# Performance work log

Hardware: AMD Instinct MI355X
Metric: run time of the kernel (lower is better)

## Reference

```python
import jax, jax.numpy as jnp
import numpy as np

N_NODES = 100000


def gcn_conv(x, edge_index, W, b):
    # PyG GCNConv: add self-loops, symmetric normalization, then scatter-add.
    n = x.shape[0]
    loops = jnp.arange(n, dtype=edge_index.dtype)
    src = jnp.concatenate([edge_index[0], loops])
    dst = jnp.concatenate([edge_index[1], loops])
    h = x @ W  # [N, F_out] -- transform before propagate (small GEMM)
    ones = jnp.ones(src.shape[0], dtype=x.dtype)
    deg = jax.ops.segment_sum(ones, dst, num_segments=n)  # in-degree incl. self-loop
    dinv = jnp.where(deg > 0, jax.lax.rsqrt(deg), 0.0)
    norm = dinv[src] * dinv[dst]  # [E+N]
    msg = h[src] * norm[:, None]  # gather + scale, [E+N, F_out]
    out = jax.ops.segment_sum(msg, dst, num_segments=n)  # scatter-add
    return out + b


def setup_inputs() -> dict:
    key = jax.random.key(0)
    k1, k2, k3, k4 = jax.random.split(key, 4)
    d = 128
    x = jax.random.normal(k1, (N_NODES, d), dtype=jnp.float32)
    edge_index = jax.random.randint(k2, (2, 1600000), 0, N_NODES, dtype=jnp.int64)
    scale = 1.0 / np.sqrt(d)
    W1 = jax.random.normal(k3, (d, d), dtype=jnp.float32) * scale
    b1 = jnp.zeros((d,), dtype=jnp.float32)
    W2 = jax.random.normal(k4, (d, d), dtype=jnp.float32) * scale
    b2 = jnp.zeros((d,), dtype=jnp.float32)
    return {"x": x, "edge_index": edge_index, "W1": W1, "b1": b1, "W2": W2, "b2": b2}


def reference(x, edge_index, W1, b1, W2, b2):
    # Layer 1: GCNConv -> relu -> dropout(eval: identity)
    h = jax.nn.relu(gcn_conv(x, edge_index, W1, b1))
    # Layer 2
    h = jax.nn.relu(gcn_conv(h, edge_index, W2, b2))
    return h
```

## Files before the change

### kernel.cpp

```cpp
#include <hip/hip_runtime.h>


#define NFEAT 128
#define BSH 7
#define MAXNB 1024
#define BCAP 4096
#define HP 72
#define YP 132
#define CH2 2048

typedef __attribute__((ext_vector_type(8))) short s8v;
typedef __attribute__((ext_vector_type(4))) float f4v;
typedef __attribute__((ext_vector_type(2))) float f2v;
typedef __attribute__((ext_vector_type(4))) uint u4v;

__device__ inline ushort f2bf(float f) {
    union { float f; uint u; } x; x.f = f;
    uint u = x.u;
    return (ushort)((u + 0x7fffu + ((u >> 16) & 1u)) >> 16);
}
__device__ inline f2v unpk(uint u) {
    union { uint u; float f; } lo, hi;
    lo.u = u << 16;
    hi.u = u & 0xffff0000u;
    return (f2v){lo.f, hi.f};
}
__device__ inline void upfma2(uint4 v, float g, f2v* a) {
    a[0] += g * unpk(v.x);
    a[1] += g * unpk(v.y);
    a[2] += g * unpk(v.z);
    a[3] += g * unpk(v.w);
}

__device__ inline void node_gather(const uint4* __restrict__ hs4,
                                   const int* __restrict__ row_ptr,
                                   const int* __restrict__ col,
                                   const float* __restrict__ dinv,
                                   int node, int sub, f2v* a) {
    uint4 vself = hs4[(size_t)node * 16 + sub];
    float dself = dinv[node];
    int s = row_ptr[node], e = row_ptr[node + 1];
    int nb = (e - s) >> 2;
    int k = s;
    if (nb > 0) {
        int c0 = col[k], c1 = col[k + 1], c2 = col[k + 2], c3 = col[k + 3];
        uint4 v0 = hs4[(size_t)c0 * 16 + sub];
        uint4 v1 = hs4[(size_t)c1 * 16 + sub];
        uint4 v2 = hs4[(size_t)c2 * 16 + sub];
        uint4 v3 = hs4[(size_t)c3 * 16 + sub];
        float g0 = dinv[c0], g1 = dinv[c1], g2 = dinv[c2], g3 = dinv[c3];
        int d0 = col[k + 4], d1 = col[k + 5], d2 = col[k + 6], d3 = col[k + 7];
        k += 8;
        upfma2(vself, dself, a);
        for (int it = 1; it < nb; ++it, k += 4) {
            uint4 w0 = hs4[(size_t)d0 * 16 + sub];
            uint4 w1 = hs4[(size_t)d1 * 16 + sub];
            uint4 w2 = hs4[(size_t)d2 * 16 + sub];
            uint4 w3 = hs4[(size_t)d3 * 16 + sub];
            float h0 = dinv[d0], h1 = dinv[d1], h2 = dinv[d2], h3 = dinv[d3];
            int t0 = col[k], t1 = col[k + 1], t2 = col[k + 2], t3 = col[k + 3];
            upfma2(v0, g0, a); upfma2(v1, g1, a); upfma2(v2, g2, a); upfma2(v3, g3, a);
            v0 = w0; v1 = w1; v2 = w2; v3 = w3;
            g0 = h0; g1 = h1; g2 = h2; g3 = h3;
            d0 = t0; d1 = t1; d2 = t2; d3 = t3;
        }
        upfma2(v0, g0, a); upfma2(v1, g1, a); upfma2(v2, g2, a); upfma2(v3, g3, a);
        k = s + nb * 4;
    } else {
        upfma2(vself, dself, a);
    }
    for (; k < e; ++k) {
        int c = col[k];
        upfma2(hs4[(size_t)c * 16 + sub], dinv[c], a);
    }
}

__device__ inline void stage_w_half(ushort* Bs, const float* __restrict__ W, int h, int t) {
#pragma unroll
    for (int i = 0; i < 8; i++) {
        int idx = t + i * 256;
        int k4 = idx >> 7;
        int n = idx & 127;
        ushort o[4];
#pragma unroll
        for (int j = 0; j < 4; j++) o[j] = f2bf(W[(h * 64 + k4 * 4 + j) * NFEAT + n]);
        uint2 pk;
        __builtin_memcpy(&pk, o, 8);
        *(uint2*)&Bs[n * HP + k4 * 4] = pk;
    }
}

__global__ __launch_bounds__(256) void k_bsort(const int* __restrict__ src,
                                               const int* __restrict__ dst,
                                               int* __restrict__ gcnt,
                                               uint* __restrict__ ebuf,
                                               int E, int NB) {
    __shared__ int cnt_[MAXNB];
    __shared__ int loff[MAXNB];
    __shared__ int gbase[MAXNB];
    __shared__ int wpart[4];
    __shared__ uint sv[CH2];
    __shared__ ushort sb[CH2];

    int t = threadIdx.x;
    int e0 = blockIdx.x * CH2;
    int m = min(CH2, E - e0);

#pragma unroll
    for (int i = t; i < MAXNB; i += 256) cnt_[i] = 0;
    __syncthreads();
    for (int e = e0 + t; e < e0 + m; e += 256) atomicAdd(&cnt_[dst[e] >> BSH], 1);
    __syncthreads();
    for (int b = t; b < NB; b += 256) {
        int c = cnt_[b];
        gbase[b] = c ? (b * BCAP + atomicAdd(&gcnt[b], c)) : 0;
    }
    int v0 = cnt_[t * 4], v1 = cnt_[t * 4 + 1], v2 = cnt_[t * 4 + 2], v3 = cnt_[t * 4 + 3];
    int my = v0 + v1 + v2 + v3;
    int lane = t & 63, wv = t >> 6;
    int sc = my;
#pragma unroll
    for (int off = 1; off < 64; off <<= 1) {
        int up = __shfl_up(sc, off, 64);
        if (lane >= off) sc += up;
    }
    if (lane == 63) wpart[wv] = sc;
    __syncthreads();
    int wbase = 0;
    for (int j = 0; j < wv; j++) wbase += wpart[j];
    int run = wbase + sc - my;
    loff[t * 4] = run; cnt_[t * 4] = run; run += v0;
    loff[t * 4 + 1] = run; cnt_[t * 4 + 1] = run; run += v1;
    loff[t * 4 + 2] = run; cnt_[t * 4 + 2] = run; run += v2;
    loff[t * 4 + 3] = run; cnt_[t * 4 + 3] = run;
    __syncthreads();
    for (int e = e0 + t; e < e0 + m; e += 256) {
        int d = dst[e];
        int b = d >> BSH;
        int p = atomicAdd(&cnt_[b], 1);
        sv[p] = ((uint)src[e] << BSH) | (uint)(d & ((1 << BSH) - 1));
        sb[p] = (ushort)b;
    }
    __syncthreads();
    for (int i = t; i < m; i += 256) {
        int b = sb[i];
        int slot = gbase[b] + (i - loff[b]);
        if (slot < (b + 1) * BCAP) ebuf[slot] = sv[i];
    }
}

template <bool ABF16>
__device__ inline void gemm_body(ushort* Bs, int bid, const void* __restrict__ Ap,
                                 const float* __restrict__ W,
                                 ushort* __restrict__ hs, int M) {
    int t = threadIdx.x;
    int w = t >> 6, l = t & 63;
    int q = l >> 4, ln = l & 15;
    int row0 = (bid * 4 + w) * 16;

    int arow = row0 + ln;
    if (arow >= M) arow = M - 1;
    s8v afr[4];
    if (ABF16) {
        const ushort* A = (const ushort*)Ap + (size_t)arow * NFEAT + q * 8;
#pragma unroll
        for (int g = 0; g < 4; g++) afr[g] = *(const s8v*)(A + g * 32);
    } else {
        const float* A = (const float*)Ap + (size_t)arow * NFEAT + q * 8;
#pragma unroll
        for (int g = 0; g < 4; g++) {
            float4 f0 = *(const float4*)(A + g * 32);
            float4 f1 = *(const float4*)(A + g * 32 + 4);
            ushort o[8] = {f2bf(f0.x), f2bf(f0.y), f2bf(f0.z), f2bf(f0.w),
                           f2bf(f1.x), f2bf(f1.y), f2bf(f1.z), f2bf(f1.w)};
            __builtin_memcpy(&afr[g], o, 16);
        }
    }

    f4v acc[8];
#pragma unroll
    for (int nt = 0; nt < 8; nt++) acc[nt] = (f4v){0.f, 0.f, 0.f, 0.f};

#pragma unroll
    for (int h = 0; h < 2; h++) {
        if (h) __syncthreads();
        stage_w_half(Bs, W, h, t);
        __syncthreads();
#pragma unroll
        for (int nt = 0; nt < 8; nt++) {
            const ushort* Bp = Bs + (nt * 16 + ln) * HP + q * 8;
#pragma unroll
            for (int ks = 0; ks < 2; ks++) {
                s8v bfr = *(const s8v*)(Bp + ks * 32);
                acc[nt] = __builtin_amdgcn_mfma_f32_16x16x32_bf16(afr[h * 2 + ks], bfr, acc[nt], 0, 0, 0);
            }
        }
    }

#pragma unroll
    for (int r = 0; r < 4; r++) {
        int row = row0 + q * 4 + r;
        if (row < M) {
            ushort* hp = hs + (size_t)row * NFEAT + ln;
#pragma unroll
            for (int nt = 0; nt < 8; nt++) hp[nt * 16] = f2bf(acc[nt][r]);
        }
    }
}

__device__ inline void fill2_body(char* smem, int b,
                                  const uint* __restrict__ ebuf,
                                  const int* __restrict__ gcnt,
                                  int* __restrict__ row_ptr,
                                  float* __restrict__ dinv,
                                  int* __restrict__ col,
                                  int N, int E, int NB) {
    int* cnt = (int*)smem;
    int* pre = cnt + 128;
    int* sred = pre + 128;
    int* colL = sred + 256;
    int t = threadIdx.x;
    int part = 0;
    for (int j = t; j < b; j += 256) part += gcnt[j];
#pragma unroll
    for (int off = 32; off >= 1; off >>= 1) part += __shfl_down(part, off, 64);
    if ((t & 63) == 0) sred[t >> 6] = part;
    __syncthreads();
    int gb = sred[0] + sred[1] + sred[2] + sred[3];
    int m = min(gcnt[b], BCAP);
    if (t < 128) cnt[t] = 0;
    __syncthreads();
    const uint* eb = ebuf + (size_t)b * BCAP;
    for (int i = t; i < m; i += 256) atomicAdd(&cnt[eb[i] & 127], 1);
    __syncthreads();
    if (t < 128) pre[t] = cnt[t];
    __syncthreads();
    for (int off = 1; off < 128; off <<= 1) {
        int add = (t >= off && t < 128) ? pre[t - off] : 0;
        __syncthreads();
        if (t < 128) pre[t] += add;
        __syncthreads();
    }
    if (t < 128) {
        pre[t] -= cnt[t];
        int node = (b << BSH) + t;
        if (node < N) {
            row_ptr[node] = gb + pre[t];
            dinv[node] = rsqrtf((float)(cnt[t] + 1));
        }
    }
    __syncthreads();
    for (int i = t; i < m; i += 256) {
        uint p = eb[i];
        int pos = atomicAdd(&pre[p & 127], 1);
        colL[pos] = (int)(p >> BSH);
    }
    __syncthreads();
    for (int i = t; i < m; i += 256) col[gb + i] = colL[i];
    if (b == NB - 1 && t == 0) row_ptr[N] = E;
}

__global__ __launch_bounds__(256) void k_fused2(const uint* __restrict__ ebuf,
                                                const int* __restrict__ gcnt,
                                                int* __restrict__ row_ptr,
                                                float* __restrict__ dinv,
                                                int* __restrict__ col,
                                                int N, int E, int NB,
                                                const float* __restrict__ x,
                                                const float* __restrict__ W1,
                                                ushort* __restrict__ hs) {
    __shared__ __align__(16) char smem[18432];
    int bid = blockIdx.x;
    int r = bid % 3;
    int fid = bid / 3;
    if (r == 0 && fid < NB) {
        fill2_body(smem, fid, ebuf, gcnt, row_ptr, dinv, col, N, E, NB);
    } else {
        int fills_before = min(fid + (r ? 1 : 0), NB);
        gemm_body<false>((ushort*)smem, bid - fills_before, x, W1, hs, N);
    }
}

__global__ __launch_bounds__(256, 4) void k_aggG(const uint4* __restrict__ hs4,
                                                 const int* __restrict__ row_ptr,
                                                 const int* __restrict__ col,
                                                 const float* __restrict__ dinv,
                                                 const float* __restrict__ bias,
                                                 const float* __restrict__ W2,
                                                 ushort* __restrict__ hs2, int N) {
    __shared__ __align__(16) ushort smem[128 * HP];
    ushort* yT = smem;
    ushort* Bs = smem;
    int t = threadIdx.x;
    int grp = t >> 4, sub = t & 15;
    int base = blockIdx.x * 64;

    const float4* b4 = (const float4*)bias;
    float4 bb0 = b4[sub * 2], bb1 = b4[sub * 2 + 1];

    for (int i = 0; i < 4; i++) {
        int myn = grp + i * 16;
        int node = base + myn;
        uint4 pk = make_uint4(0, 0, 0, 0);
        if (node < N) {
            f2v a[4];
#pragma unroll
            for (int j = 0; j < 4; j++) a[j] = (f2v){0.f, 0.f};
            node_gather(hs4, row_ptr, col, dinv, node, sub, a);
            float di = dinv[node];
            ushort o[8];
            o[0] = f2bf(fmaxf(fmaf(di, a[0].x, bb0.x), 0.f));
            o[1] = f2bf(fmaxf(fmaf(di, a[0].y, bb0.y), 0.f));
            o[2] = f2bf(fmaxf(fmaf(di, a[1].x, bb0.z), 0.f));
            o[3] = f2bf(fmaxf(fmaf(di, a[1].y, bb0.w), 0.f));
            o[4] = f2bf(fmaxf(fmaf(di, a[2].x, bb1.x), 0.f));
            o[5] = f2bf(fmaxf(fmaf(di, a[2].y, bb1.y), 0.f));
            o[6] = f2bf(fmaxf(fmaf(di, a[3].x, bb1.z), 0.f));
            o[7] = f2bf(fmaxf(fmaf(di, a[3].y, bb1.w), 0.f));
            __builtin_memcpy(&pk, o, 16);
        }
        *(uint4*)&yT[myn * YP + sub * 8] = pk;
    }
    __syncthreads();

    int w = t >> 6, l = t & 63;
    int q = l >> 4, ln = l & 15;
    s8v a2[4];
#pragma unroll
    for (int g = 0; g < 4; g++)
        a2[g] = *(const s8v*)&yT[(w * 16 + ln) * YP + g * 32 + q * 8];
    __syncthreads();

    f4v acc[8];
#pragma unroll
    for (int nt = 0; nt < 8; nt++) acc[nt] = (f4v){0.f, 0.f, 0.f, 0.f};
#pragma unroll
    for (int h = 0; h < 2; h++) {
        if (h) __syncthreads();
        stage_w_half(Bs, W2, h, t);
        __syncthreads();
#pragma unroll
        for (int nt = 0; nt < 8; nt++) {
            const ushort* Bp = Bs + (nt * 16 + ln) * HP + q * 8;
#pragma unroll
            for (int ks = 0; ks < 2; ks++) {
                s8v bfr = *(const s8v*)(Bp + ks * 32);
                acc[nt] = __builtin_amdgcn_mfma_f32_16x16x32_bf16(a2[h * 2 + ks], bfr, acc[nt], 0, 0, 0);
            }
        }
    }
#pragma unroll
    for (int rr = 0; rr < 4; rr++) {
        int node = base + w * 16 + q * 4 + rr;
        if (node < N) {
            ushort* hp = hs2 + (size_t)node * NFEAT + ln;
#pragma unroll
            for (int nt = 0; nt < 8; nt++) hp[nt * 16] = f2bf(acc[nt][rr]);
        }
    }
}

template <bool OUT_BF16>
__global__ __launch_bounds__(256) void k_aggregate(const uint4* __restrict__ hs4,
                                                   const int* __restrict__ row_ptr,
                                                   const int* __restrict__ col,
                                                   const float* __restrict__ dinv,
                                                   const float* __restrict__ bias,
                                                   void* __restrict__ outp, int N) {
    int node = blockIdx.x * 16 + (threadIdx.x >> 4);
    if (node >= N) return;
    int sub = threadIdx.x & 15;

    f2v a[4];
#pragma unroll
    for (int j = 0; j < 4; j++) a[j] = (f2v){0.f, 0.f};
    node_gather(hs4, row_ptr, col, dinv, node, sub, a);

    float di = dinv[node];
    const float4* b4 = (const float4*)bias;
    float4 b0 = b4[sub * 2], b1 = b4[sub * 2 + 1];
    float r[8];
    r[0] = fmaxf(fmaf(di, a[0].x, b0.x), 0.f);
    r[1] = fmaxf(fmaf(di, a[0].y, b0.y), 0.f);
    r[2] = fmaxf(fmaf(di, a[1].x, b0.z), 0.f);
    r[3] = fmaxf(fmaf(di, a[1].y, b0.w), 0.f);
    r[4] = fmaxf(fmaf(di, a[2].x, b1.x), 0.f);
    r[5] = fmaxf(fmaf(di, a[2].y, b1.y), 0.f);
    r[6] = fmaxf(fmaf(di, a[3].x, b1.z), 0.f);
    r[7] = fmaxf(fmaf(di, a[3].y, b1.w), 0.f);
    if (OUT_BF16) {
        ushort o[8];
#pragma unroll
        for (int j = 0; j < 8; j++) o[j] = f2bf(r[j]);
        u4v pk;
        __builtin_memcpy(&pk, o, 16);
        __builtin_nontemporal_store(pk, (u4v*)outp + (size_t)node * 16 + sub);
    } else {
        float* orow = (float*)outp + (size_t)node * NFEAT + sub * 8;
        f4v r0 = {r[0], r[1], r[2], r[3]};
        f4v r1 = {r[4], r[5], r[6], r[7]};
        __builtin_nontemporal_store(r0, (f4v*)orow);
        __builtin_nontemporal_store(r1, (f4v*)(orow + 4));
    }
}

extern "C" void kernel_launch(void* const* d_in, const int* in_sizes, int n_in,
                              void* d_out, int out_size, void* d_ws, size_t ws_size,
                              hipStream_t stream) {
    const float* x = (const float*)d_in[0];
    const int* ei = (const int*)d_in[1];
    const float* W1 = (const float*)d_in[2];
    const float* b1 = (const float*)d_in[3];
    const float* W2 = (const float*)d_in[4];
    const float* b2 = (const float*)d_in[5];
    float* out = (float*)d_out;

    const int N = in_sizes[0] / NFEAT;
    const int E = in_sizes[1] / 2;
    const int* src = ei;
    const int* dst = ei + E;
    const int NB = (N + (1 << BSH) - 1) >> BSH;

    char* w = (char*)d_ws;
    size_t off = 0;
    auto alloc = [&](size_t bytes) -> void* {
        void* p = w + off;
        off = (off + bytes + 511) & ~(size_t)511;
        return p;
    };
    ushort* hs = (ushort*)alloc((size_t)N * NFEAT * 2);
    ushort* hs2 = (ushort*)alloc((size_t)N * NFEAT * 2);
    int* row_ptr = (int*)alloc((size_t)(N + 1) * 4);
    float* dinv = (float*)alloc((size_t)N * 4);
    int* col = (int*)alloc((size_t)(E + 64) * 4);
    uint* ebuf = (uint*)alloc((size_t)NB * BCAP * 4);
    int* gcnt = (int*)alloc((size_t)MAXNB * 4);
    (void)ws_size; (void)n_in; (void)out_size;

    const int sortBlk = (E + CH2 - 1) / CH2;
    const int gemmBlk = (N + 63) / 64;
    const int aggBlk = (N + 15) / 16;

    hipMemsetAsync(gcnt, 0, (size_t)MAXNB * 4, stream);
    k_bsort<<<sortBlk, 256, 0, stream>>>(src, dst, gcnt, ebuf, E, NB);
    k_fused2<<<NB + gemmBlk, 256, 0, stream>>>(ebuf, gcnt, row_ptr, dinv, col, N, E, NB,
                                               x, W1, hs);
    k_aggG<<<gemmBlk, 256, 0, stream>>>((const uint4*)hs, row_ptr, col, dinv, b1, W2, hs2, N);
    k_aggregate<false><<<aggBlk, 256, 0, stream>>>((const uint4*)hs2, row_ptr, col, dinv, b2, out, N);
}
```

Measured before the change: 306.0 us.

## Drop global CSR build; sort bucket halves in LDS inside aggregation kernels

Removes the separate CSR fill pass (row_ptr, col, dinv) and instead has each aggregation block locally sort its half-bucket of edges into LDS, with a small atomic degree kernel feeding the source-side normalization. The source-side dinv scaling is folded into the GEMM epilogue, so the gather does plain adds with no per-neighbor dinv loads. The bucket sort now runs fused alongside the first GEMM. In exchange each of the two aggregation kernels re-reads and re-sorts ebuf, a global atomic degree pass is added, and per-half neighbor lists are capped at 2048 entries.

Result: slower. 357.9 us (+16.9%).

```diff
diff --git a/kernel.cpp b/kernel.cpp
--- a/kernel.cpp
+++ b/kernel.cpp
@@ -8,6 +8,7 @@
 #define HP 72
 #define YP 132
 #define CH2 2048
+#define CLCAP 2064
 
 typedef __attribute__((ext_vector_type(8))) short s8v;
 typedef __attribute__((ext_vector_type(4))) float f4v;
@@ -25,54 +26,81 @@
     hi.u = u & 0xffff0000u;
     return (f2v){lo.f, hi.f};
 }
-__device__ inline void upfma2(uint4 v, float g, f2v* a) {
-    a[0] += g * unpk(v.x);
-    a[1] += g * unpk(v.y);
-    a[2] += g * unpk(v.z);
-    a[3] += g * unpk(v.w);
-}
-
-__device__ inline void node_gather(const uint4* __restrict__ hs4,
-                                   const int* __restrict__ row_ptr,
-                                   const int* __restrict__ col,
-                                   const float* __restrict__ dinv,
-                                   int node, int sub, f2v* a) {
+__device__ inline void upadd2(uint4 v, f2v* a) {
+    a[0] += unpk(v.x);
+    a[1] += unpk(v.y);
+    a[2] += unpk(v.z);
+    a[3] += unpk(v.w);
+}
+
+__device__ inline void node_gather_lds(const uint4* __restrict__ hs4,
+                                       const int* colL, int s, int e,
+                                       int node, int sub, f2v* a) {
     uint4 vself = hs4[(size_t)node * 16 + sub];
-    float dself = dinv[node];
-    int s = row_ptr[node], e = row_ptr[node + 1];
     int nb = (e - s) >> 2;
     int k = s;
     if (nb > 0) {
-        int c0 = col[k], c1 = col[k + 1], c2 = col[k + 2], c3 = col[k + 3];
+        int c0 = colL[k], c1 = colL[k + 1], c2 = colL[k + 2], c3 = colL[k + 3];
         uint4 v0 = hs4[(size_t)c0 * 16 + sub];
         uint4 v1 = hs4[(size_t)c1 * 16 + sub];
         uint4 v2 = hs4[(size_t)c2 * 16 + sub];
         uint4 v3 = hs4[(size_t)c3 * 16 + sub];
-        float g0 = dinv[c0], g1 = dinv[c1], g2 = dinv[c2], g3 = dinv[c3];
-        int d0 = col[k + 4], d1 = col[k + 5], d2 = col[k + 6], d3 = col[k + 7];
+        int d0 = colL[k + 4], d1 = colL[k + 5], d2 = colL[k + 6], d3 = colL[k + 7];
         k += 8;
-        upfma2(vself, dself, a);
+        upadd2(vself, a);
         for (int it = 1; it < nb; ++it, k += 4) {
             uint4 w0 = hs4[(size_t)d0 * 16 + sub];
             uint4 w1 = hs4[(size_t)d1 * 16 + sub];
             uint4 w2 = hs4[(size_t)d2 * 16 + sub];
             uint4 w3 = hs4[(size_t)d3 * 16 + sub];
-            float h0 = dinv[d0], h1 = dinv[d1], h2 = dinv[d2], h3 = dinv[d3];
-            int t0 = col[k], t1 = col[k + 1], t2 = col[k + 2], t3 = col[k + 3];
-            upfma2(v0, g0, a); upfma2(v1, g1, a); upfma2(v2, g2, a); upfma2(v3, g3, a);
+            int t0 = colL[k], t1 = colL[k + 1], t2 = colL[k + 2], t3 = colL[k + 3];
+            upadd2(v0, a); upadd2(v1, a); upadd2(v2, a); upadd2(v3, a);
             v0 = w0; v1 = w1; v2 = w2; v3 = w3;
-            g0 = h0; g1 = h1; g2 = h2; g3 = h3;
             d0 = t0; d1 = t1; d2 = t2; d3 = t3;
         }
-        upfma2(v0, g0, a); upfma2(v1, g1, a); upfma2(v2, g2, a); upfma2(v3, g3, a);
+        upadd2(v0, a); upadd2(v1, a); upadd2(v2, a); upadd2(v3, a);
         k = s + nb * 4;
     } else {
-        upfma2(vself, dself, a);
-    }
-    for (; k < e; ++k) {
-        int c = col[k];
-        upfma2(hs4[(size_t)c * 16 + sub], dinv[c], a);
-    }
+        upadd2(vself, a);
+    }
+    for (; k < e; ++k) upadd2(hs4[(size_t)colL[k] * 16 + sub], a);
+}
+
+__device__ inline void half_sort(const uint* __restrict__ ebuf,
+                                 const int* __restrict__ gcnt,
+                                 int b, int half, int* cnt, int* sstart, int* pre,
+                                 int* colL) {
+    int t = threadIdx.x;
+    int m = min(gcnt[b], BCAP);
+    const uint* eb = ebuf + (size_t)b * BCAP;
+    if (t < 64) cnt[t] = 0;
+    __syncthreads();
+    for (int i = t; i < m; i += 256) {
+        int low = (int)(eb[i] & 127u);
+        if ((low >> 6) == half) atomicAdd(&cnt[low & 63], 1);
+    }
+    __syncthreads();
+    if (t < 64) {
+        int v = cnt[t];
+        int sc = v;
+#pragma unroll
+        for (int off = 1; off < 64; off <<= 1) {
+            int u = __shfl_up(sc, off, 64);
+            if (t >= off) sc += u;
+        }
+        sstart[t] = sc - v;
+        pre[t] = sc - v;
+    }
+    __syncthreads();
+    for (int i = t; i < m; i += 256) {
+        uint p = eb[i];
+        int low = (int)(p & 127u);
+        if ((low >> 6) == half) {
+            int pos = atomicAdd(&pre[low & 63], 1);
+            if (pos < 2048) colL[pos] = (int)(p >> BSH);
+        }
+    }
+    __syncthreads();
 }
 
 __device__ inline void stage_w_half(ushort* Bs, const float* __restrict__ W, int h, int t) {
@@ -90,20 +118,36 @@
     }
 }
 
-__global__ __launch_bounds__(256) void k_bsort(const int* __restrict__ src,
-                                               const int* __restrict__ dst,
-                                               int* __restrict__ gcnt,
-                                               uint* __restrict__ ebuf,
-                                               int E, int NB) {
-    __shared__ int cnt_[MAXNB];
-    __shared__ int loff[MAXNB];
-    __shared__ int gbase[MAXNB];
-    __shared__ int wpart[4];
-    __shared__ uint sv[CH2];
-    __shared__ ushort sb[CH2];
+__global__ __launch_bounds__(256) void k_deg(const int* __restrict__ dst,
+                                             int* __restrict__ deg, int E) {
+    int i = blockIdx.x * 256 + threadIdx.x;
+    int stride = gridDim.x * 256;
+    int E4 = E >> 2;
+    const int4* d4 = (const int4*)dst;
+    for (int k = i; k < E4; k += stride) {
+        int4 v = d4[k];
+        atomicAdd(&deg[v.x], 1);
+        atomicAdd(&deg[v.y], 1);
+        atomicAdd(&deg[v.z], 1);
+        atomicAdd(&deg[v.w], 1);
+    }
+    for (int k = E4 * 4 + i; k < E; k += stride) atomicAdd(&deg[dst[k]], 1);
+}
+
+__device__ inline void bsort_body(char* smem, int sid,
+                                  const int* __restrict__ src,
+                                  const int* __restrict__ dst,
+                                  int* __restrict__ gcnt,
+                                  uint* __restrict__ ebuf, int E, int NB) {
+    int* cnt_ = (int*)smem;
+    int* loff = cnt_ + MAXNB;
+    int* gbase = loff + MAXNB;
+    int* wpart = gbase + MAXNB;
+    uint* sv = (uint*)(wpart + 4);
+    ushort* sb = (ushort*)(sv + CH2);
 
     int t = threadIdx.x;
-    int e0 = blockIdx.x * CH2;
+    int e0 = sid * CH2;
     int m = min(CH2, E - e0);
 
 #pragma unroll
@@ -149,10 +193,10 @@
     }
 }
 
-template <bool ABF16>
-__device__ inline void gemm_body(ushort* Bs, int bid, const void* __restrict__ Ap,
-                                 const float* __restrict__ W,
-                                 ushort* __restrict__ hs, int M) {
+__device__ inline void gemm_body_f32(ushort* Bs, int bid, const float* __restrict__ Ap,
+                                     const float* __restrict__ W,
+                                     const int* __restrict__ deg,
+                                     ushort* __restrict__ hs, int M) {
     int t = threadIdx.x;
     int w = t >> 6, l = t & 63;
     int q = l >> 4, ln = l & 15;
@@ -161,20 +205,14 @@
     int arow = row0 + ln;
     if (arow >= M) arow = M - 1;
     s8v afr[4];
-    if (ABF16) {
-        const ushort* A = (const ushort*)Ap + (size_t)arow * NFEAT + q * 8;
-#pragma unroll
-        for (int g = 0; g < 4; g++) afr[g] = *(const s8v*)(A + g * 32);
-    } else {
-        const float* A = (const float*)Ap + (size_t)arow * NFEAT + q * 8;
-#pragma unroll
-        for (int g = 0; g < 4; g++) {
-            float4 f0 = *(const float4*)(A + g * 32);
-            float4 f1 = *(const float4*)(A + g * 32 + 4);
-            ushort o[8] = {f2bf(f0.x), f2bf(f0.y), f2bf(f0.z), f2bf(f0.w),
-                           f2bf(f1.x), f2bf(f1.y), f2bf(f1.z), f2bf(f1.w)};
-            __builtin_memcpy(&afr[g], o, 16);
-        }
+    const float* A = Ap + (size_t)arow * NFEAT + q * 8;
+#pragma unroll
+    for (int g = 0; g < 4; g++) {
+        float4 f0 = *(const float4*)(A + g * 32);
+        float4 f1 = *(const float4*)(A + g * 32 + 4);
+        ushort o[8] = {f2bf(f0.x), f2bf(f0.y), f2bf(f0.z), f2bf(f0.w),
+                       f2bf(f1.x), f2bf(f1.y), f2bf(f1.z), f2bf(f1.w)};
+        __builtin_memcpy(&afr[g], o, 16);
     }
 
     f4v acc[8];
@@ -201,113 +239,71 @@
     for (int r = 0; r < 4; r++) {
         int row = row0 + q * 4 + r;
         if (row < M) {
+            float sc = rsqrtf((float)(deg[row] + 1));
             ushort* hp = hs + (size_t)row * NFEAT + ln;
 #pragma unroll
-            for (int nt = 0; nt < 8; nt++) hp[nt * 16] = f2bf(acc[nt][r]);
-        }
-    }
-}
-
-__device__ inline void fill2_body(char* smem, int b,
-                                  const uint* __restrict__ ebuf,
-                                  const int* __restrict__ gcnt,
-                                  int* __restrict__ row_ptr,
-                                  float* __restrict__ dinv,
-                                  int* __restrict__ col,
-                                  int N, int E, int NB) {
-    int* cnt = (int*)smem;
-    int* pre = cnt + 128;
-    int* sred = pre + 128;
-    int* colL = sred + 256;
-    int t = threadIdx.x;
-    int part = 0;
-    for (int j = t; j < b; j += 256) part += gcnt[j];
-#pragma unroll
-    for (int off = 32; off >= 1; off >>= 1) part += __shfl_down(part, off, 64);
-    if ((t & 63) == 0) sred[t >> 6] = part;
-    __syncthreads();
-    int gb = sred[0] + sred[1] + sred[2] + sred[3];
-    int m = min(gcnt[b], BCAP);
-    if (t < 128) cnt[t] = 0;
-    __syncthreads();
-    const uint* eb = ebuf + (size_t)b * BCAP;
-    for (int i = t; i < m; i += 256) atomicAdd(&cnt[eb[i] & 127], 1);
-    __syncthreads();
-    if (t < 128) pre[t] = cnt[t];
-    __syncthreads();
-    for (int off = 1; off < 128; off <<= 1) {
-        int add = (t >= off && t < 128) ? pre[t - off] : 0;
-        __syncthreads();
-        if (t < 128) pre[t] += add;
-        __syncthreads();
-    }
-    if (t < 128) {
-        pre[t] -= cnt[t];
-        int node = (b << BSH) + t;
-        if (node < N) {
-            row_ptr[node] = gb + pre[t];
-            dinv[node] = rsqrtf((float)(cnt[t] + 1));
-        }
-    }
-    __syncthreads();
-    for (int i = t; i < m; i += 256) {
-        uint p = eb[i];
-        int pos = atomicAdd(&pre[p & 127], 1);
-        colL[pos] = (int)(p >> BSH);
-    }
-    __syncthreads();
-    for (int i = t; i < m; i += 256) col[gb + i] = colL[i];
-    if (b == NB - 1 && t == 0) row_ptr[N] = E;
-}
-
-__global__ __launch_bounds__(256) void k_fused2(const uint* __restrict__ ebuf,
-                                                const int* __restrict__ gcnt,
-                                                int* __restrict__ row_ptr,
-                                                float* __restrict__ dinv,
-                                                int* __restrict__ col,
-                                                int N, int E, int NB,
+            for (int nt = 0; nt < 8; nt++) hp[nt * 16] = f2bf(acc[nt][r] * sc);
+        }
+    }
+}
+
+__global__ __launch_bounds__(256) void k_fusedA(const int* __restrict__ src,
+                                                const int* __restrict__ dst,
+                                                int* __restrict__ gcnt,
+                                                uint* __restrict__ ebuf,
+                                                int E, int NB, int chBlk,
                                                 const float* __restrict__ x,
                                                 const float* __restrict__ W1,
-                                                ushort* __restrict__ hs) {
-    __shared__ __align__(16) char smem[18432];
+                                                const int* __restrict__ deg,
+                                                ushort* __restrict__ hs, int M) {
+    __shared__ __align__(16) char smem[24592];
     int bid = blockIdx.x;
-    int r = bid % 3;
-    int fid = bid / 3;
-    if (r == 0 && fid < NB) {
-        fill2_body(smem, fid, ebuf, gcnt, row_ptr, dinv, col, N, E, NB);
+    int sid = bid / 3, r = bid % 3;
+    if (r == 0 && sid < chBlk) {
+        bsort_body(smem, sid, src, dst, gcnt, ebuf, E, NB);
     } else {
-        int fills_before = min(fid + (r ? 1 : 0), NB);
-        gemm_body<false>((ushort*)smem, bid - fills_before, x, W1, hs, N);
-    }
-}
-
-__global__ __launch_bounds__(256, 4) void k_aggG(const uint4* __restrict__ hs4,
-                                                 const int* __restrict__ row_ptr,
-                                                 const int* __restrict__ col,
-                                                 const float* __restrict__ dinv,
-                                                 const float* __restrict__ bias,
-                                                 const float* __restrict__ W2,
-                                                 ushort* __restrict__ hs2, int N) {
-    __shared__ __align__(16) ushort smem[128 * HP];
-    ushort* yT = smem;
-    ushort* Bs = smem;
+        int sorts_before = min(sid + (r ? 1 : 0), chBlk);
+        gemm_body_f32((ushort*)smem, bid - sorts_before, x, W1, deg, hs, M);
+    }
+}
+
+__global__ __launch_bounds__(256, 4) void k_aggB1(const uint4* __restrict__ hs4,
+                                                  const uint* __restrict__ ebuf,
+                                                  const int* __restrict__ gcnt,
+                                                  const float* __restrict__ bias,
+                                                  const float* __restrict__ W2,
+                                                  ushort* __restrict__ hs2, int N) {
+    __shared__ __align__(16) char smem[36096];
+    ushort* yT = (ushort*)smem;
+    char* scr = smem + 16896;
+    int* cnt = (int*)(smem + 35328);
+    int* sstart = (int*)(smem + 35584);
+    int* pre = (int*)(smem + 35840);
+    int* colL = (int*)scr;
+    ushort* Bs = (ushort*)scr;
+
     int t = threadIdx.x;
+    int b = blockIdx.x >> 1, half = blockIdx.x & 1;
+    int base = (b << BSH) + half * 64;
+
+    half_sort(ebuf, gcnt, b, half, cnt, sstart, pre, colL);
+
     int grp = t >> 4, sub = t & 15;
-    int base = blockIdx.x * 64;
-
     const float4* b4 = (const float4*)bias;
     float4 bb0 = b4[sub * 2], bb1 = b4[sub * 2 + 1];
 
     for (int i = 0; i < 4; i++) {
-        int myn = grp + i * 16;
-        int node = base + myn;
+        int lo = grp + i * 16;
+        int node = base + lo;
         uint4 pk = make_uint4(0, 0, 0, 0);
         if (node < N) {
             f2v a[4];
 #pragma unroll
             for (int j = 0; j < 4; j++) a[j] = (f2v){0.f, 0.f};
-            node_gather(hs4, row_ptr, col, dinv, node, sub, a);
-            float di = dinv[node];
+            int s = sstart[lo];
+            int e = min(s + cnt[lo], 2048);
+            node_gather_lds(hs4, colL, s, e, node, sub, a);
+            float di = rsqrtf((float)(cnt[lo] + 1));
             ushort o[8];
             o[0] = f2bf(fmaxf(fmaf(di, a[0].x, bb0.x), 0.f));
             o[1] = f2bf(fmaxf(fmaf(di, a[0].y, bb0.y), 0.f));
@@ -319,7 +315,7 @@
             o[7] = f2bf(fmaxf(fmaf(di, a[3].y, bb1.w), 0.f));
             __builtin_memcpy(&pk, o, 16);
         }
-        *(uint4*)&yT[myn * YP + sub * 8] = pk;
+        *(uint4*)&yT[lo * YP + sub * 8] = pk;
     }
     __syncthreads();
 
@@ -329,7 +325,6 @@
 #pragma unroll
     for (int g = 0; g < 4; g++)
         a2[g] = *(const s8v*)&yT[(w * 16 + ln) * YP + g * 32 + q * 8];
-    __syncthreads();
 
     f4v acc[8];
 #pragma unroll
@@ -351,52 +346,58 @@
     }
 #pragma unroll
     for (int rr = 0; rr < 4; rr++) {
-        int node = base + w * 16 + q * 4 + rr;
+        int lrow = w * 16 + q * 4 + rr;
+        int node = base + lrow;
         if (node < N) {
+            float sc = rsqrtf((float)(cnt[lrow] + 1));
             ushort* hp = hs2 + (size_t)node * NFEAT + ln;
 #pragma unroll
-            for (int nt = 0; nt < 8; nt++) hp[nt * 16] = f2bf(acc[nt][rr]);
-        }
-    }
-}
-
-template <bool OUT_BF16>
-__global__ __launch_bounds__(256) void k_aggregate(const uint4* __restrict__ hs4,
-                                                   const int* __restrict__ row_ptr,
-                                                   const int* __restrict__ col,
-                                                   const float* __restrict__ dinv,
-                                                   const float* __restrict__ bias,
-                                                   void* __restrict__ outp, int N) {
-    int node = blockIdx.x * 16 + (threadIdx.x >> 4);
-    if (node >= N) return;
-    int sub = threadIdx.x & 15;
-
-    f2v a[4];
-#pragma unroll
-    for (int j = 0; j < 4; j++) a[j] = (f2v){0.f, 0.f};
-    node_gather(hs4, row_ptr, col, dinv, node, sub, a);
-
-    float di = dinv[node];
+            for (int nt = 0; nt < 8; nt++) hp[nt * 16] = f2bf(acc[nt][rr] * sc);
+        }
+    }
+}
+
+__global__ __launch_bounds__(256, 6) void k_aggB2(const uint4* __restrict__ hs4,
+                                                  const uint* __restrict__ ebuf,
+                                                  const int* __restrict__ gcnt,
+                                                  const float* __restrict__ bias,
+                                                  float* __restrict__ outp, int N) {
+    __shared__ int cnt[64];
+    __shared__ int sstart[64];
+    __shared__ int pre[64];
+    __shared__ int colL[CLCAP];
+
+    int t = threadIdx.x;
+    int b = blockIdx.x >> 1, half = blockIdx.x & 1;
+    int base = (b << BSH) + half * 64;
+
+    half_sort(ebuf, gcnt, b, half, cnt, sstart, pre, colL);
+
+    int grp = t >> 4, sub = t & 15;
     const float4* b4 = (const float4*)bias;
-    float4 b0 = b4[sub * 2], b1 = b4[sub * 2 + 1];
-    float r[8];
-    r[0] = fmaxf(fmaf(di, a[0].x, b0.x), 0.f);
-    r[1] = fmaxf(fmaf(di, a[0].y, b0.y), 0.f);
-    r[2] = fmaxf(fmaf(di, a[1].x, b0.z), 0.f);
-    r[3] = fmaxf(fmaf(di, a[1].y, b0.w), 0.f);
-    r[4] = fmaxf(fmaf(di, a[2].x, b1.x), 0.f);
-    r[5] = fmaxf(fmaf(di, a[2].y, b1.y), 0.f);
-    r[6] = fmaxf(fmaf(di, a[3].x, b1.z), 0.f);
-    r[7] = fmaxf(fmaf(di, a[3].y, b1.w), 0.f);
-    if (OUT_BF16) {
-        ushort o[8];
-#pragma unroll
-        for (int j = 0; j < 8; j++) o[j] = f2bf(r[j]);
-        u4v pk;
-        __builtin_memcpy(&pk, o, 16);
-        __builtin_nontemporal_store(pk, (u4v*)outp + (size_t)node * 16 + sub);
-    } else {
-        float* orow = (float*)outp + (size_t)node * NFEAT + sub * 8;
+    float4 bb0 = b4[sub * 2], bb1 = b4[sub * 2 + 1];
+
+    for (int i = 0; i < 4; i++) {
+        int lo = grp + i * 16;
+        int node = base + lo;
+        if (node >= N) continue;
+        f2v a[4];
+#pragma unroll
+        for (int j = 0; j < 4; j++) a[j] = (f2v){0.f, 0.f};
+        int s = sstart[lo];
+        int e = min(s + cnt[lo], 2048);
+        node_gather_lds(hs4, colL, s, e, node, sub, a);
+        float di = rsqrtf((float)(cnt[lo] + 1));
+        float r[8];
+        r[0] = fmaxf(fmaf(di, a[0].x, bb0.x), 0.f);
+        r[1] = fmaxf(fmaf(di, a[0].y, bb0.y), 0.f);
+        r[2] = fmaxf(fmaf(di, a[1].x, bb0.z), 0.f);
+        r[3] = fmaxf(fmaf(di, a[1].y, bb0.w), 0.f);
+        r[4] = fmaxf(fmaf(di, a[2].x, bb1.x), 0.f);
+        r[5] = fmaxf(fmaf(di, a[2].y, bb1.y), 0.f);
+        r[6] = fmaxf(fmaf(di, a[3].x, bb1.z), 0.f);
+        r[7] = fmaxf(fmaf(di, a[3].y, bb1.w), 0.f);
+        float* orow = outp + (size_t)node * NFEAT + sub * 8;
         f4v r0 = {r[0], r[1], r[2], r[3]};
         f4v r1 = {r[4], r[5], r[6], r[7]};
         __builtin_nontemporal_store(r0, (f4v*)orow);
@@ -430,21 +431,20 @@
     };
     ushort* hs = (ushort*)alloc((size_t)N * NFEAT * 2);
     ushort* hs2 = (ushort*)alloc((size_t)N * NFEAT * 2);
-    int* row_ptr = (int*)alloc((size_t)(N + 1) * 4);
-    float* dinv = (float*)alloc((size_t)N * 4);
-    int* col = (int*)alloc((size_t)(E + 64) * 4);
+    int* deg = (int*)alloc((size_t)N * 4);
     uint* ebuf = (uint*)alloc((size_t)NB * BCAP * 4);
     int* gcnt = (int*)alloc((size_t)MAXNB * 4);
     (void)ws_size; (void)n_in; (void)out_size;
 
     const int sortBlk = (E + CH2 - 1) / CH2;
     const int gemmBlk = (N + 63) / 64;
-    const int aggBlk = (N + 15) / 16;
-
+    const int aggBlk = 2 * NB;
+
+    hipMemsetAsync(deg, 0, (size_t)N * 4, stream);
     hipMemsetAsync(gcnt, 0, (size_t)MAXNB * 4, stream);
-    k_bsort<<<sortBlk, 256, 0, stream>>>(src, dst, gcnt, ebuf, E, NB);
-    k_fused2<<<NB + gemmBlk, 256, 0, stream>>>(ebuf, gcnt, row_ptr, dinv, col, N, E, NB,
-                                               x, W1, hs);
-    k_aggG<<<gemmBlk, 256, 0, stream>>>((const uint4*)hs, row_ptr, col, dinv, b1, W2, hs2, N);
-    k_aggregate<false><<<aggBlk, 256, 0, stream>>>((const uint4*)hs2, row_ptr, col, dinv, b2, out, N);
-}
+    k_deg<<<1024, 256, 0, stream>>>(dst, deg, E);
+    k_fusedA<<<sortBlk + gemmBlk, 256, 0, stream>>>(src, dst, gcnt, ebuf, E, NB, sortBlk,
+                                                    x, W1, deg, hs, N);
+    k_aggB1<<<aggBlk, 256, 0, stream>>>((const uint4*)hs, ebuf, gcnt, b1, W2, hs2, N);
+    k_aggB2<<<aggBlk, 256, 0, stream>>>((const uint4*)hs2, ebuf, gcnt, b2, out, N);
+}
```
